# Optimization experiments

Hardware: AMD Instinct MI355X
Metric: run time of the kernel (lower is better)

The kernel has to match this reference:

```python
import jax, jax.numpy as jnp
import numpy as np

FEAT = 2048
NUM_CLASSES = 751
EPS = 1e-5


def setup_inputs() -> dict:
    key = jax.random.key(0)
    k1, k2, k3 = jax.random.split(key, 3)
    probe_x = jax.random.normal(k1, (64, FEAT), dtype=jnp.float32)
    gallery_x = jax.random.normal(k2, (256, FEAT), dtype=jnp.float32)
    # BatchNorm1d affine params (PyTorch init: gamma=1, beta=0)
    bn_gamma = jnp.ones((FEAT,), dtype=jnp.float32)
    bn_beta = jnp.zeros((FEAT,), dtype=jnp.float32)
    # classifier: weight ~ N(0, 0.001), bias = 0
    W = jax.random.normal(k3, (NUM_CLASSES, FEAT), dtype=jnp.float32) * 0.001
    b = jnp.zeros((NUM_CLASSES,), dtype=jnp.float32)
    return {"probe_x": probe_x, "gallery_x": gallery_x,
            "bn_gamma": bn_gamma, "bn_beta": bn_beta, "W": W, "b": b}


def reference(probe_x, gallery_x, bn_gamma, bn_beta, W, b):
    n_probe, feat = probe_x.shape
    n_gallery = gallery_x.shape[0]
    # broadcast squared difference: [Np, Ng, F]
    diff = jnp.square(probe_x[:, None, :] - gallery_x[None, :, :])
    d = diff.reshape(n_probe * n_gallery, feat)
    # BatchNorm1d in training mode: biased batch statistics over the batch dim
    mean = jnp.mean(d, axis=0)
    var = jnp.mean(jnp.square(d - mean), axis=0)
    bn = (d - mean) * (bn_gamma / jnp.sqrt(var + EPS)) + bn_beta
    # Linear classifier
    cls = jnp.einsum('nf,cf->nc', bn, W) + b
    return cls.reshape(n_probe, n_gallery, -1)
```

## Files before the change

### kernel.cpp

```cpp
#include <hip/hip_runtime.h>
#include <hip/hip_bf16.h>
#include <hip/hip_fp16.h>

#define FEAT 2048
#define NCLS 751
#define NPAD 768
#define NPRB 64
#define NGAL 256
#define WSCALE 256.0f

typedef _Float16 f16x8 __attribute__((ext_vector_type(8)));
typedef float f32x4 __attribute__((ext_vector_type(4)));

__device__ __forceinline__ unsigned short f2h_u(float x) {
  union { _Float16 h; unsigned short u; } v;
  v.h = (_Float16)x;
  return v.u;
}

__global__ void stats_kernel(const float* __restrict__ P, const float* __restrict__ G,
                             const float* __restrict__ gamma, const float* __restrict__ beta,
                             float* __restrict__ st) {
  int fx = threadIdx.x & 31, ry = threadIdx.x >> 5;
  int f = blockIdx.x * 32 + fx;
  float a1 = 0, a2 = 0, a3 = 0, a4 = 0;
  for (int r = ry; r < NPRB; r += 8) {
    float x = P[r * FEAT + f], x2 = x * x;
    a1 += x; a2 += x2; a3 += x2 * x; a4 += x2 * x2;
  }
  float b1 = 0, b2 = 0, b3 = 0, b4 = 0;
  for (int r = ry; r < NGAL; r += 8) {
    float x = G[r * FEAT + f], x2 = x * x;
    b1 += x; b2 += x2; b3 += x2 * x; b4 += x2 * x2;
  }
  __shared__ float red[8][8][32];
  float vals[8] = {a1, a2, a3, a4, b1, b2, b3, b4};
#pragma unroll
  for (int m = 0; m < 8; ++m) red[m][ry][fx] = vals[m];
  __syncthreads();
  if (ry == 0) {
    float mm[8];
#pragma unroll
    for (int m = 0; m < 8; ++m) {
      float sum = 0.f;
#pragma unroll
      for (int r = 0; r < 8; ++r) sum += red[m][r][fx];
      mm[m] = sum;
    }
    float M1p = mm[0] * (1.f / NPRB), M2p = mm[1] * (1.f / NPRB);
    float M3p = mm[2] * (1.f / NPRB), M4p = mm[3] * (1.f / NPRB);
    float M1g = mm[4] * (1.f / NGAL), M2g = mm[5] * (1.f / NGAL);
    float M3g = mm[6] * (1.f / NGAL), M4g = mm[7] * (1.f / NGAL);
    float mean = M2p - 2.f * M1p * M1g + M2g;
    float Ed2 = M4p - 4.f * M3p * M1g + 6.f * M2p * M2g - 4.f * M1p * M3g + M4g;
    float var = Ed2 - mean * mean;
    float sv = gamma[f] / sqrtf(var + 1e-5f);
    st[f] = sv;
    st[FEAT + f] = beta[f] - mean * sv;
  }
}

__global__ void prepw_kernel(const float* __restrict__ W, const float* __restrict__ b,
                             const float* __restrict__ st,
                             unsigned short* __restrict__ Wp, float* __restrict__ bp) {
  int c = blockIdx.x;
  int f = threadIdx.x * 8;
  float4 w0 = make_float4(0.f, 0.f, 0.f, 0.f), w1 = w0;
  if (c < NCLS) {
    const float4* wsrc = (const float4*)(W + (size_t)c * FEAT + f);
    w0 = wsrc[0]; w1 = wsrc[1];
  }
  const float4* s4 = (const float4*)(st + f);
  float4 s0 = s4[0], s1 = s4[1];
  const float4* t4 = (const float4*)(st + FEAT + f);
  float4 t0 = t4[0], t1 = t4[1];
  uint4 u;
  u.x = (unsigned int)f2h_u(w0.x * s0.x * WSCALE) | ((unsigned int)f2h_u(w0.y * s0.y * WSCALE) << 16);
  u.y = (unsigned int)f2h_u(w0.z * s0.z * WSCALE) | ((unsigned int)f2h_u(w0.w * s0.w * WSCALE) << 16);
  u.z = (unsigned int)f2h_u(w1.x * s1.x * WSCALE) | ((unsigned int)f2h_u(w1.y * s1.y * WSCALE) << 16);
  u.w = (unsigned int)f2h_u(w1.z * s1.z * WSCALE) | ((unsigned int)f2h_u(w1.w * s1.w * WSCALE) << 16);
  *(uint4*)(Wp + (size_t)c * FEAT + f) = u;
  float acc = t0.x * w0.x + t0.y * w0.y + t0.z * w0.z + t0.w * w0.w +
              t1.x * w1.x + t1.y * w1.y + t1.z * w1.z + t1.w * w1.w;
#pragma unroll
  for (int off = 32; off > 0; off >>= 1) acc += __shfl_down(acc, off, 64);
  __shared__ float r[4];
  int wave = threadIdx.x >> 6, lane = threadIdx.x & 63;
  if (lane == 0) r[wave] = acc;
  __syncthreads();
  if (threadIdx.x == 0) bp[c] = (c < NCLS ? b[c] : 0.f) + r[0] + r[1] + r[2] + r[3];
}

__global__ __launch_bounds__(256, 3)
void gemm_fused_kernel(const float* __restrict__ P, const float* __restrict__ G,
                       const unsigned short* __restrict__ Wp,
                       const float* __restrict__ bp, float* __restrict__ out) {
  __shared__ unsigned short As[128 * 64];
  __shared__ unsigned short Bs[128 * 64];
  __shared__ float Ps[FEAT];

  const int tid = threadIdx.x;
  const int lane = tid & 63, wave = tid >> 6;
  const int mtile = blockIdx.x, ntile = blockIdx.y;
  const int p = mtile >> 1;

  const int srow = tid >> 3;
  const int sch = (tid & 7) ^ (srow & 7);
  const float* gp = G + (size_t)((mtile & 1) * 128 + srow) * FEAT + sch * 8;
  const unsigned short* bg = Wp + (size_t)(ntile * 128 + srow) * FEAT + sch * 8;
  unsigned short* asw = As + srow * 64 + (tid & 7) * 8;
  char* blds = (char*)Bs + wave * 1024;

  {
    const float4* psrc = (const float4*)(P + (size_t)p * FEAT) + tid * 2;
    float4 pa = psrc[0], pb = psrc[1];
    float4* pd = (float4*)Ps + tid * 2;
    pd[0] = pa; pd[1] = pb;
  }
  float4 g0[4], g1[4];
#pragma unroll
  for (int j = 0; j < 4; ++j) {
    const float4* gs = (const float4*)(gp + (size_t)j * 32 * FEAT);
    g0[j] = gs[0]; g1[j] = gs[1];
  }

  f32x4 acc[4][4];
#pragma unroll
  for (int mi = 0; mi < 4; ++mi)
#pragma unroll
    for (int ni = 0; ni < 4; ++ni) acc[mi][ni] = (f32x4){0.f, 0.f, 0.f, 0.f};

  const int wm = (wave & 1) * 64, wn = (wave >> 1) * 64;
  const int frow = lane & 15, fsw = lane & 7, fk = lane >> 4;

  __syncthreads();

  for (int k0 = 0; k0 < FEAT; k0 += 64) {
#pragma unroll
    for (int j = 0; j < 4; ++j)
      __builtin_amdgcn_global_load_lds(
          (const __attribute__((address_space(1))) void*)(bg + k0 + (size_t)j * 32 * FEAT),
          (__attribute__((address_space(3))) void*)(blds + j * 4096), 16, 0, 0);

    const float* pr = Ps + k0 + sch * 8;
    float4 p0 = *(const float4*)pr;
    float4 p1 = *(const float4*)(pr + 4);
#pragma unroll
    for (int j = 0; j < 4; ++j) {
      float d0 = p0.x - g0[j].x, d1 = p0.y - g0[j].y;
      float d2 = p0.z - g0[j].z, d3 = p0.w - g0[j].w;
      float d4 = p1.x - g1[j].x, d5 = p1.y - g1[j].y;
      float d6 = p1.z - g1[j].z, d7 = p1.w - g1[j].w;
      uint4 u;
      u.x = (unsigned int)f2h_u(d0 * d0) | ((unsigned int)f2h_u(d1 * d1) << 16);
      u.y = (unsigned int)f2h_u(d2 * d2) | ((unsigned int)f2h_u(d3 * d3) << 16);
      u.z = (unsigned int)f2h_u(d4 * d4) | ((unsigned int)f2h_u(d5 * d5) << 16);
      u.w = (unsigned int)f2h_u(d6 * d6) | ((unsigned int)f2h_u(d7 * d7) << 16);
      *(uint4*)(asw + j * 32 * 64) = u;
    }
    __syncthreads();

    if (k0 + 64 < FEAT) {
#pragma unroll
      for (int j = 0; j < 4; ++j) {
        const float4* gs = (const float4*)(gp + k0 + 64 + (size_t)j * 32 * FEAT);
        g0[j] = gs[0]; g1[j] = gs[1];
      }
    }

#pragma unroll
    for (int kk = 0; kk < 2; ++kk) {
      const int slot = (kk * 4 + fk) ^ fsw;
      f16x8 af[4], bf[4];
#pragma unroll
      for (int mi = 0; mi < 4; ++mi)
        af[mi] = *(const f16x8*)(As + (wm + mi * 16 + frow) * 64 + slot * 8);
#pragma unroll
      for (int ni = 0; ni < 4; ++ni)
        bf[ni] = *(const f16x8*)(Bs + (wn + ni * 16 + frow) * 64 + slot * 8);
#pragma unroll
      for (int mi = 0; mi < 4; ++mi)
#pragma unroll
        for (int ni = 0; ni < 4; ++ni)
          acc[mi][ni] = __builtin_amdgcn_mfma_f32_16x16x32_f16(af[mi], bf[ni], acc[mi][ni], 0, 0, 0);
    }
    __syncthreads();
  }

  const int col0 = ntile * 128 + wn + (lane & 15);
  const int row0 = mtile * 128 + wm + ((lane >> 4) << 2);
#pragma unroll
  for (int ni = 0; ni < 4; ++ni) {
    int col = col0 + ni * 16;
    if (col >= NCLS) continue;
    float bv = bp[col];
#pragma unroll
    for (int mi = 0; mi < 4; ++mi) {
      int row = row0 + mi * 16;
#pragma unroll
      for (int r = 0; r < 4; ++r)
        out[(size_t)(row + r) * NCLS + col] = acc[mi][ni][r] * (1.0f / WSCALE) + bv;
    }
  }
}

extern "C" void kernel_launch(void* const* d_in, const int* in_sizes, int n_in,
                              void* d_out, int out_size, void* d_ws, size_t ws_size,
                              hipStream_t stream) {
  const float* P = (const float*)d_in[0];
  const float* G = (const float*)d_in[1];
  const float* gamma = (const float*)d_in[2];
  const float* beta = (const float*)d_in[3];
  const float* W = (const float*)d_in[4];
  const float* b = (const float*)d_in[5];
  float* out = (float*)d_out;

  float* st = (float*)d_ws;
  float* bp = st + 2 * FEAT;
  unsigned short* Wp = (unsigned short*)(bp + NPAD);

  hipLaunchKernelGGL(stats_kernel, dim3(64), dim3(256), 0, stream, P, G, gamma, beta, st);
  hipLaunchKernelGGL(prepw_kernel, dim3(NPAD), dim3(256), 0, stream, W, b, st, Wp, bp);
  hipLaunchKernelGGL(gemm_fused_kernel, dim3(128, 6), dim3(256), 0, stream, P, G, Wp, bp, out);
}
```

Measured before the change: 173.0 us.

## Double-buffer A and B tiles in LDS to overlap loads with MFMA

Converts the GEMM main loop to a double-buffered pipeline. The next W tile is issued as a direct global-to-LDS load, and the next squared-difference A tile is built into the alternate buffer while MFMAs run on the current one. This cuts the syncs per iteration from two to one, and s_setprio raises wave priority around the MFMA block. In exchange, LDS use doubles to about 72KB, so the launch bound drops from 3 to 2 blocks per CU and occupancy falls.

```diff
diff --git a/kernel.cpp b/kernel.cpp
--- a/kernel.cpp
+++ b/kernel.cpp
@@ -91,12 +91,12 @@
   if (threadIdx.x == 0) bp[c] = (c < NCLS ? b[c] : 0.f) + r[0] + r[1] + r[2] + r[3];
 }
 
-__global__ __launch_bounds__(256, 3)
+__global__ __launch_bounds__(256, 2)
 void gemm_fused_kernel(const float* __restrict__ P, const float* __restrict__ G,
                        const unsigned short* __restrict__ Wp,
                        const float* __restrict__ bp, float* __restrict__ out) {
-  __shared__ unsigned short As[128 * 64];
-  __shared__ unsigned short Bs[128 * 64];
+  __shared__ unsigned short As[2][128 * 64];
+  __shared__ unsigned short Bs[2][128 * 64];
   __shared__ float Ps[FEAT];
 
   const int tid = threadIdx.x;
@@ -108,8 +108,8 @@
   const int sch = (tid & 7) ^ (srow & 7);
   const float* gp = G + (size_t)((mtile & 1) * 128 + srow) * FEAT + sch * 8;
   const unsigned short* bg = Wp + (size_t)(ntile * 128 + srow) * FEAT + sch * 8;
-  unsigned short* asw = As + srow * 64 + (tid & 7) * 8;
-  char* blds = (char*)Bs + wave * 1024;
+  const int aswo = srow * 64 + (tid & 7) * 8;
+  const int bldo = wave * 1024;
 
   {
     const float4* psrc = (const float4*)(P + (size_t)p * FEAT) + tid * 2;
@@ -117,32 +117,21 @@
     float4* pd = (float4*)Ps + tid * 2;
     pd[0] = pa; pd[1] = pb;
   }
+#pragma unroll
+  for (int j = 0; j < 4; ++j)
+    __builtin_amdgcn_global_load_lds(
+        (const __attribute__((address_space(1))) void*)(bg + (size_t)j * 32 * FEAT),
+        (__attribute__((address_space(3))) void*)((char*)Bs[0] + bldo + j * 4096), 16, 0, 0);
   float4 g0[4], g1[4];
 #pragma unroll
   for (int j = 0; j < 4; ++j) {
     const float4* gs = (const float4*)(gp + (size_t)j * 32 * FEAT);
     g0[j] = gs[0]; g1[j] = gs[1];
   }
-
-  f32x4 acc[4][4];
-#pragma unroll
-  for (int mi = 0; mi < 4; ++mi)
-#pragma unroll
-    for (int ni = 0; ni < 4; ++ni) acc[mi][ni] = (f32x4){0.f, 0.f, 0.f, 0.f};
-
-  const int wm = (wave & 1) * 64, wn = (wave >> 1) * 64;
-  const int frow = lane & 15, fsw = lane & 7, fk = lane >> 4;
-
-  __syncthreads();
-
-  for (int k0 = 0; k0 < FEAT; k0 += 64) {
-#pragma unroll
-    for (int j = 0; j < 4; ++j)
-      __builtin_amdgcn_global_load_lds(
-          (const __attribute__((address_space(1))) void*)(bg + k0 + (size_t)j * 32 * FEAT),
-          (__attribute__((address_space(3))) void*)(blds + j * 4096), 16, 0, 0);
-
-    const float* pr = Ps + k0 + sch * 8;
+  __syncthreads();
+
+  {
+    const float* pr = Ps + sch * 8;
     float4 p0 = *(const float4*)pr;
     float4 p1 = *(const float4*)(pr + 4);
 #pragma unroll
@@ -156,35 +145,79 @@
       u.y = (unsigned int)f2h_u(d2 * d2) | ((unsigned int)f2h_u(d3 * d3) << 16);
       u.z = (unsigned int)f2h_u(d4 * d4) | ((unsigned int)f2h_u(d5 * d5) << 16);
       u.w = (unsigned int)f2h_u(d6 * d6) | ((unsigned int)f2h_u(d7 * d7) << 16);
-      *(uint4*)(asw + j * 32 * 64) = u;
-    }
-    __syncthreads();
-
-    if (k0 + 64 < FEAT) {
+      *(uint4*)(As[0] + aswo + j * 32 * 64) = u;
+    }
+  }
+  __syncthreads();
+
+  f32x4 acc[4][4];
+#pragma unroll
+  for (int mi = 0; mi < 4; ++mi)
+#pragma unroll
+    for (int ni = 0; ni < 4; ++ni) acc[mi][ni] = (f32x4){0.f, 0.f, 0.f, 0.f};
+
+  const int wm = (wave & 1) * 64, wn = (wave >> 1) * 64;
+  const int frow = lane & 15, fsw = lane & 7, fk = lane >> 4;
+
+  int cur = 0;
+  for (int t = 0; t < 32; ++t) {
+    const int k0 = t * 64;
+    const bool has_next = (t < 31);
+    float4 p0n, p1n;
+
+    if (has_next) {
 #pragma unroll
       for (int j = 0; j < 4; ++j) {
         const float4* gs = (const float4*)(gp + k0 + 64 + (size_t)j * 32 * FEAT);
         g0[j] = gs[0]; g1[j] = gs[1];
       }
-    }
-
+#pragma unroll
+      for (int j = 0; j < 4; ++j)
+        __builtin_amdgcn_global_load_lds(
+            (const __attribute__((address_space(1))) void*)(bg + k0 + 64 + (size_t)j * 32 * FEAT),
+            (__attribute__((address_space(3))) void*)((char*)Bs[cur ^ 1] + bldo + j * 4096), 16, 0, 0);
+      const float* prn = Ps + k0 + 64 + sch * 8;
+      p0n = *(const float4*)prn;
+      p1n = *(const float4*)(prn + 4);
+    }
+
+    __builtin_amdgcn_s_setprio(1);
 #pragma unroll
     for (int kk = 0; kk < 2; ++kk) {
       const int slot = (kk * 4 + fk) ^ fsw;
       f16x8 af[4], bf[4];
 #pragma unroll
       for (int mi = 0; mi < 4; ++mi)
-        af[mi] = *(const f16x8*)(As + (wm + mi * 16 + frow) * 64 + slot * 8);
+        af[mi] = *(const f16x8*)(As[cur] + (wm + mi * 16 + frow) * 64 + slot * 8);
 #pragma unroll
       for (int ni = 0; ni < 4; ++ni)
-        bf[ni] = *(const f16x8*)(Bs + (wn + ni * 16 + frow) * 64 + slot * 8);
+        bf[ni] = *(const f16x8*)(Bs[cur] + (wn + ni * 16 + frow) * 64 + slot * 8);
 #pragma unroll
       for (int mi = 0; mi < 4; ++mi)
 #pragma unroll
         for (int ni = 0; ni < 4; ++ni)
           acc[mi][ni] = __builtin_amdgcn_mfma_f32_16x16x32_f16(af[mi], bf[ni], acc[mi][ni], 0, 0, 0);
     }
+    __builtin_amdgcn_s_setprio(0);
+
+    if (has_next) {
+#pragma unroll
+      for (int j = 0; j < 4; ++j) {
+        float d0 = p0n.x - g0[j].x, d1 = p0n.y - g0[j].y;
+        float d2 = p0n.z - g0[j].z, d3 = p0n.w - g0[j].w;
+        float d4 = p1n.x - g1[j].x, d5 = p1n.y - g1[j].y;
+        float d6 = p1n.z - g1[j].z, d7 = p1n.w - g1[j].w;
+        uint4 u;
+        u.x = (unsigned int)f2h_u(d0 * d0) | ((unsigned int)f2h_u(d1 * d1) << 16);
+        u.y = (unsigned int)f2h_u(d2 * d2) | ((unsigned int)f2h_u(d3 * d3) << 16);
+        u.z = (unsigned int)f2h_u(d4 * d4) | ((unsigned int)f2h_u(d5 * d5) << 16);
+        u.w = (unsigned int)f2h_u(d6 * d6) | ((unsigned int)f2h_u(d7 * d7) << 16);
+        *(uint4*)(As[cur ^ 1] + aswo + j * 32 * 64) = u;
+      }
+    }
+
     __syncthreads();
+    cur ^= 1;
   }
 
   const int col0 = ntile * 128 + wn + (lane & 15);
```

New measurement: 204.7 us. +18.3%, slower.

## Double-buffer GEMM LDS tiles with K=32 steps and widen stats kernel grid

Applied to the files above, without the earlier changes.

The fused GEMM now uses double-buffered LDS tiles of depth 32 instead of a single 64-deep tile. The next tile's W async load and A-tile squared-difference compute are issued around the MFMA block, which is wrapped in s_setprio, so each K-step needs one barrier instead of two. The stats kernel now spreads 8 features per block over 256 blocks with a two-level shared reduction, giving more parallelism for the moment sums. This trades more loop iterations and LDS swizzle changes for overlap of loads and conversion with matrix math.

```diff
diff --git a/kernel.cpp b/kernel.cpp
--- a/kernel.cpp
+++ b/kernel.cpp
@@ -18,35 +18,44 @@
   return v.u;
 }
 
-__global__ void stats_kernel(const float* __restrict__ P, const float* __restrict__ G,
-                             const float* __restrict__ gamma, const float* __restrict__ beta,
-                             float* __restrict__ st) {
-  int fx = threadIdx.x & 31, ry = threadIdx.x >> 5;
-  int f = blockIdx.x * 32 + fx;
+__global__ __launch_bounds__(256)
+void stats_kernel(const float* __restrict__ P, const float* __restrict__ G,
+                  const float* __restrict__ gamma, const float* __restrict__ beta,
+                  float* __restrict__ st) {
+  const int t = threadIdx.x;
+  const int fx = t & 7, ry = t >> 3;
+  const int f = blockIdx.x * 8 + fx;
   float a1 = 0, a2 = 0, a3 = 0, a4 = 0;
-  for (int r = ry; r < NPRB; r += 8) {
+#pragma unroll
+  for (int r = ry; r < NPRB; r += 32) {
     float x = P[r * FEAT + f], x2 = x * x;
     a1 += x; a2 += x2; a3 += x2 * x; a4 += x2 * x2;
   }
   float b1 = 0, b2 = 0, b3 = 0, b4 = 0;
-  for (int r = ry; r < NGAL; r += 8) {
+#pragma unroll
+  for (int r = ry; r < NGAL; r += 32) {
     float x = G[r * FEAT + f], x2 = x * x;
     b1 += x; b2 += x2; b3 += x2 * x; b4 += x2 * x2;
   }
-  __shared__ float red[8][8][32];
+  __shared__ float red[8][32][8];
+  __shared__ float red2[8][4][8];
   float vals[8] = {a1, a2, a3, a4, b1, b2, b3, b4};
 #pragma unroll
   for (int m = 0; m < 8; ++m) red[m][ry][fx] = vals[m];
   __syncthreads();
-  if (ry == 0) {
+  {
+    int m = t >> 5, q = (t >> 3) & 3, fx2 = t & 7;
+    float s = 0.f;
+#pragma unroll
+    for (int r = 0; r < 8; ++r) s += red[m][q * 8 + r][fx2];
+    red2[m][q][fx2] = s;
+  }
+  __syncthreads();
+  if (t < 8) {
     float mm[8];
 #pragma unroll
-    for (int m = 0; m < 8; ++m) {
-      float sum = 0.f;
-#pragma unroll
-      for (int r = 0; r < 8; ++r) sum += red[m][r][fx];
-      mm[m] = sum;
-    }
+    for (int m = 0; m < 8; ++m)
+      mm[m] = red2[m][0][t] + red2[m][1][t] + red2[m][2][t] + red2[m][3][t];
     float M1p = mm[0] * (1.f / NPRB), M2p = mm[1] * (1.f / NPRB);
     float M3p = mm[2] * (1.f / NPRB), M4p = mm[3] * (1.f / NPRB);
     float M1g = mm[4] * (1.f / NGAL), M2g = mm[5] * (1.f / NGAL);
@@ -54,9 +63,10 @@
     float mean = M2p - 2.f * M1p * M1g + M2g;
     float Ed2 = M4p - 4.f * M3p * M1g + 6.f * M2p * M2g - 4.f * M1p * M3g + M4g;
     float var = Ed2 - mean * mean;
-    float sv = gamma[f] / sqrtf(var + 1e-5f);
-    st[f] = sv;
-    st[FEAT + f] = beta[f] - mean * sv;
+    int ff = blockIdx.x * 8 + t;
+    float sv = gamma[ff] / sqrtf(var + 1e-5f);
+    st[ff] = sv;
+    st[FEAT + ff] = beta[ff] - mean * sv;
   }
 }
 
@@ -95,34 +105,62 @@
 void gemm_fused_kernel(const float* __restrict__ P, const float* __restrict__ G,
                        const unsigned short* __restrict__ Wp,
                        const float* __restrict__ bp, float* __restrict__ out) {
-  __shared__ unsigned short As[128 * 64];
-  __shared__ unsigned short Bs[128 * 64];
-  __shared__ float Ps[FEAT];
+  __shared__ unsigned short As[2][128 * 32];
+  __shared__ unsigned short Bs[2][128 * 32];
+  __shared__ float Ps[3072];
 
   const int tid = threadIdx.x;
   const int lane = tid & 63, wave = tid >> 6;
   const int mtile = blockIdx.x, ntile = blockIdx.y;
   const int p = mtile >> 1;
 
-  const int srow = tid >> 3;
-  const int sch = (tid & 7) ^ (srow & 7);
-  const float* gp = G + (size_t)((mtile & 1) * 128 + srow) * FEAT + sch * 8;
-  const unsigned short* bg = Wp + (size_t)(ntile * 128 + srow) * FEAT + sch * 8;
-  unsigned short* asw = As + srow * 64 + (tid & 7) * 8;
-  char* blds = (char*)Bs + wave * 1024;
+  const int arow = tid >> 1, ah = tid & 1;
+  const float* gp = G + (size_t)((mtile & 1) * 128 + arow) * FEAT + ah * 16;
+  const int aslot0 = (2 * ah) ^ (arow & 3);
+
+  const int brow = tid >> 2;
+  const int bch = (tid & 3) ^ (brow & 3);
+  const unsigned short* bg = Wp + (size_t)(ntile * 128 + brow) * FEAT + bch * 8;
+  const int bldo = wave * 1024;
 
   {
     const float4* psrc = (const float4*)(P + (size_t)p * FEAT) + tid * 2;
     float4 pa = psrc[0], pb = psrc[1];
-    float4* pd = (float4*)Ps + tid * 2;
-    pd[0] = pa; pd[1] = pb;
-  }
-  float4 g0[4], g1[4];
-#pragma unroll
-  for (int j = 0; j < 4; ++j) {
-    const float4* gs = (const float4*)(gp + (size_t)j * 32 * FEAT);
-    g0[j] = gs[0]; g1[j] = gs[1];
-  }
+    ((float4*)Ps)[tid * 2] = pa;
+    ((float4*)Ps)[tid * 2 + 1] = pb;
+  }
+  float4 g[4];
+#pragma unroll
+  for (int j = 0; j < 4; ++j) g[j] = ((const float4*)gp)[j];
+#pragma unroll
+  for (int j = 0; j < 2; ++j)
+    __builtin_amdgcn_global_load_lds(
+        (const __attribute__((address_space(1))) void*)(bg + (size_t)j * 64 * FEAT),
+        (__attribute__((address_space(3))) void*)((char*)Bs[0] + j * 4096 + bldo), 16, 0, 0);
+  __syncthreads();
+
+  {
+    const float* pr = Ps + ah * 16;
+    float4 p0 = ((const float4*)pr)[0], p1 = ((const float4*)pr)[1];
+    float4 p2 = ((const float4*)pr)[2], p3 = ((const float4*)pr)[3];
+    float d0 = p0.x - g[0].x, d1 = p0.y - g[0].y, d2 = p0.z - g[0].z, d3 = p0.w - g[0].w;
+    float d4 = p1.x - g[1].x, d5 = p1.y - g[1].y, d6 = p1.z - g[1].z, d7 = p1.w - g[1].w;
+    float e0 = p2.x - g[2].x, e1 = p2.y - g[2].y, e2 = p2.z - g[2].z, e3 = p2.w - g[2].w;
+    float e4 = p3.x - g[3].x, e5 = p3.y - g[3].y, e6 = p3.z - g[3].z, e7 = p3.w - g[3].w;
+    uint4 ua, ub;
+    ua.x = (unsigned int)f2h_u(d0 * d0) | ((unsigned int)f2h_u(d1 * d1) << 16);
+    ua.y = (unsigned int)f2h_u(d2 * d2) | ((unsigned int)f2h_u(d3 * d3) << 16);
+    ua.z = (unsigned int)f2h_u(d4 * d4) | ((unsigned int)f2h_u(d5 * d5) << 16);
+    ua.w = (unsigned int)f2h_u(d6 * d6) | ((unsigned int)f2h_u(d7 * d7) << 16);
+    ub.x = (unsigned int)f2h_u(e0 * e0) | ((unsigned int)f2h_u(e1 * e1) << 16);
+    ub.y = (unsigned int)f2h_u(e2 * e2) | ((unsigned int)f2h_u(e3 * e3) << 16);
+    ub.z = (unsigned int)f2h_u(e4 * e4) | ((unsigned int)f2h_u(e5 * e5) << 16);
+    ub.w = (unsigned int)f2h_u(e6 * e6) | ((unsigned int)f2h_u(e7 * e7) << 16);
+    unsigned short* ab = As[0] + arow * 32;
+    *(uint4*)(ab + aslot0 * 8) = ua;
+    *(uint4*)(ab + (aslot0 ^ 1) * 8) = ub;
+  }
+  __syncthreads();
 
   f32x4 acc[4][4];
 #pragma unroll
@@ -131,60 +169,67 @@
     for (int ni = 0; ni < 4; ++ni) acc[mi][ni] = (f32x4){0.f, 0.f, 0.f, 0.f};
 
   const int wm = (wave & 1) * 64, wn = (wave >> 1) * 64;
-  const int frow = lane & 15, fsw = lane & 7, fk = lane >> 4;
-
-  __syncthreads();
-
-  for (int k0 = 0; k0 < FEAT; k0 += 64) {
-#pragma unroll
-    for (int j = 0; j < 4; ++j)
-      __builtin_amdgcn_global_load_lds(
-          (const __attribute__((address_space(1))) void*)(bg + k0 + (size_t)j * 32 * FEAT),
-          (__attribute__((address_space(3))) void*)(blds + j * 4096), 16, 0, 0);
-
-    const float* pr = Ps + k0 + sch * 8;
-    float4 p0 = *(const float4*)pr;
-    float4 p1 = *(const float4*)(pr + 4);
-#pragma unroll
-    for (int j = 0; j < 4; ++j) {
-      float d0 = p0.x - g0[j].x, d1 = p0.y - g0[j].y;
-      float d2 = p0.z - g0[j].z, d3 = p0.w - g0[j].w;
-      float d4 = p1.x - g1[j].x, d5 = p1.y - g1[j].y;
-      float d6 = p1.z - g1[j].z, d7 = p1.w - g1[j].w;
-      uint4 u;
-      u.x = (unsigned int)f2h_u(d0 * d0) | ((unsigned int)f2h_u(d1 * d1) << 16);
-      u.y = (unsigned int)f2h_u(d2 * d2) | ((unsigned int)f2h_u(d3 * d3) << 16);
-      u.z = (unsigned int)f2h_u(d4 * d4) | ((unsigned int)f2h_u(d5 * d5) << 16);
-      u.w = (unsigned int)f2h_u(d6 * d6) | ((unsigned int)f2h_u(d7 * d7) << 16);
-      *(uint4*)(asw + j * 32 * 64) = u;
-    }
-    __syncthreads();
-
-    if (k0 + 64 < FEAT) {
-#pragma unroll
-      for (int j = 0; j < 4; ++j) {
-        const float4* gs = (const float4*)(gp + k0 + 64 + (size_t)j * 32 * FEAT);
-        g0[j] = gs[0]; g1[j] = gs[1];
-      }
-    }
-
-#pragma unroll
-    for (int kk = 0; kk < 2; ++kk) {
-      const int slot = (kk * 4 + fk) ^ fsw;
+  const int frow = lane & 15, fk = lane >> 4;
+  const int fslot = fk ^ (frow & 3);
+
+  int cur = 0;
+  for (int t = 0; t < 64; ++t) {
+    const int k0 = t * 32;
+    const bool hn = (t < 63);
+    float4 pn0, pn1, pn2, pn3;
+
+    if (hn) {
+      const float* gn = gp + k0 + 32;
+#pragma unroll
+      for (int j = 0; j < 4; ++j) g[j] = ((const float4*)gn)[j];
+#pragma unroll
+      for (int j = 0; j < 2; ++j)
+        __builtin_amdgcn_global_load_lds(
+            (const __attribute__((address_space(1))) void*)(bg + k0 + 32 + (size_t)j * 64 * FEAT),
+            (__attribute__((address_space(3))) void*)((char*)Bs[cur ^ 1] + j * 4096 + bldo), 16, 0, 0);
+      const float* prn = Ps + k0 + 32 + ah * 16;
+      pn0 = ((const float4*)prn)[0]; pn1 = ((const float4*)prn)[1];
+      pn2 = ((const float4*)prn)[2]; pn3 = ((const float4*)prn)[3];
+    }
+
+    __builtin_amdgcn_s_setprio(1);
+    {
       f16x8 af[4], bf[4];
 #pragma unroll
       for (int mi = 0; mi < 4; ++mi)
-        af[mi] = *(const f16x8*)(As + (wm + mi * 16 + frow) * 64 + slot * 8);
+        af[mi] = *(const f16x8*)(As[cur] + (wm + mi * 16 + frow) * 32 + fslot * 8);
 #pragma unroll
       for (int ni = 0; ni < 4; ++ni)
-        bf[ni] = *(const f16x8*)(Bs + (wn + ni * 16 + frow) * 64 + slot * 8);
+        bf[ni] = *(const f16x8*)(Bs[cur] + (wn + ni * 16 + frow) * 32 + fslot * 8);
 #pragma unroll
       for (int mi = 0; mi < 4; ++mi)
 #pragma unroll
         for (int ni = 0; ni < 4; ++ni)
           acc[mi][ni] = __builtin_amdgcn_mfma_f32_16x16x32_f16(af[mi], bf[ni], acc[mi][ni], 0, 0, 0);
     }
+    __builtin_amdgcn_s_setprio(0);
+
+    if (hn) {
+      float d0 = pn0.x - g[0].x, d1 = pn0.y - g[0].y, d2 = pn0.z - g[0].z, d3 = pn0.w - g[0].w;
+      float d4 = pn1.x - g[1].x, d5 = pn1.y - g[1].y, d6 = pn1.z - g[1].z, d7 = pn1.w - g[1].w;
+      float e0 = pn2.x - g[2].x, e1 = pn2.y - g[2].y, e2 = pn2.z - g[2].z, e3 = pn2.w - g[2].w;
+      float e4 = pn3.x - g[3].x, e5 = pn3.y - g[3].y, e6 = pn3.z - g[3].z, e7 = pn3.w - g[3].w;
+      uint4 ua, ub;
+      ua.x = (unsigned int)f2h_u(d0 * d0) | ((unsigned int)f2h_u(d1 * d1) << 16);
+      ua.y = (unsigned int)f2h_u(d2 * d2) | ((unsigned int)f2h_u(d3 * d3) << 16);
+      ua.z = (unsigned int)f2h_u(d4 * d4) | ((unsigned int)f2h_u(d5 * d5) << 16);
+      ua.w = (unsigned int)f2h_u(d6 * d6) | ((unsigned int)f2h_u(d7 * d7) << 16);
+      ub.x = (unsigned int)f2h_u(e0 * e0) | ((unsigned int)f2h_u(e1 * e1) << 16);
+      ub.y = (unsigned int)f2h_u(e2 * e2) | ((unsigned int)f2h_u(e3 * e3) << 16);
+      ub.z = (unsigned int)f2h_u(e4 * e4) | ((unsigned int)f2h_u(e5 * e5) << 16);
+      ub.w = (unsigned int)f2h_u(e6 * e6) | ((unsigned int)f2h_u(e7 * e7) << 16);
+      unsigned short* ab = As[cur ^ 1] + arow * 32;
+      *(uint4*)(ab + aslot0 * 8) = ua;
+      *(uint4*)(ab + (aslot0 ^ 1) * 8) = ub;
+    }
+
     __syncthreads();
+    cur ^= 1;
   }
 
   const int col0 = ntile * 128 + wn + (lane & 15);
@@ -219,7 +264,7 @@
   float* bp = st + 2 * FEAT;
   unsigned short* Wp = (unsigned short*)(bp + NPAD);
 
-  hipLaunchKernelGGL(stats_kernel, dim3(64), dim3(256), 0, stream, P, G, gamma, beta, st);
+  hipLaunchKernelGGL(stats_kernel, dim3(256), dim3(256), 0, stream, P, G, gamma, beta, st);
   hipLaunchKernelGGL(prepw_kernel, dim3(NPAD), dim3(256), 0, stream, W, b, st, Wp, bp);
   hipLaunchKernelGGL(gemm_fused_kernel, dim3(128, 6), dim3(256), 0, stream, P, G, Wp, bp, out);
 }
```

Result: no change. 170.0 us (-1.7%).
